# Kernel tuning notes

Hardware: AMD Instinct MI355X
Metric: run time of the kernel (lower is better)

Reference implementation:

```python
import jax, jax.numpy as jnp
import numpy as np

N = 1000000
E = 16000000


def gcn_conv(x, W, b, src, dst, dinv_sqrt):
    # x: [N, Cin]; W: [Cin, Cout]; src/dst: [E'] (self-loops included)
    xw = x @ W                                   # [N, Cout]
    norm = dinv_sqrt[src] * dinv_sqrt[dst]       # [E']
    msg = xw[src] * norm[:, None]                # [E', Cout]
    out = jax.ops.segment_sum(msg, dst, num_segments=x.shape[0])
    return out + b


def setup_inputs() -> dict:
    key = jax.random.key(0)
    ks = jax.random.split(key, 8)
    x = jax.random.normal(ks[0], (N, 1), dtype=jnp.float32)
    edge_index = jax.random.randint(ks[1], (2, E), 0, N, dtype=jnp.int64)
    W1 = jax.random.normal(ks[2], (1, 3), dtype=jnp.float32)
    b1 = jax.random.normal(ks[3], (3,), dtype=jnp.float32) * 0.1
    W2 = jax.random.normal(ks[4], (3, 3), dtype=jnp.float32) * 0.5
    b2 = jax.random.normal(ks[5], (3,), dtype=jnp.float32) * 0.1
    W3 = jax.random.normal(ks[6], (3, 3), dtype=jnp.float32) * 0.5
    b3 = jax.random.normal(ks[7], (3,), dtype=jnp.float32) * 0.1
    return {"x": x, "edge_index": edge_index, "W1": W1, "b1": b1,
            "W2": W2, "b2": b2, "W3": W3, "b3": b3}


def reference(x, edge_index, W1, b1, W2, b2, W3, b3):
    n = x.shape[0]
    # add self-loops (PyG GCNConv default)
    loop = jnp.arange(n, dtype=edge_index.dtype)
    src = jnp.concatenate([edge_index[0], loop])
    dst = jnp.concatenate([edge_index[1], loop])
    # symmetric normalization: deg over targets of A + I
    deg = jax.ops.segment_sum(jnp.ones_like(dst, dtype=x.dtype), dst, num_segments=n)
    dinv_sqrt = jnp.where(deg > 0, jax.lax.rsqrt(deg), 0.0)
    h = jax.nn.relu(gcn_conv(x, W1, b1, src, dst, dinv_sqrt))
    h = jax.nn.relu(gcn_conv(h, W2, b2, src, dst, dinv_sqrt))
    h = jax.nn.relu(gcn_conv(h, W3, b3, src, dst, dinv_sqrt))
    return h
```

## Files before the change

kernel.cpp:

```cpp
#include <hip/hip_runtime.h>

#define THREADS 256
#define SCAN_TPB 256
#define SCAN_ELEMS 4096
#define CHUNK 16384
#define BUCKET_BITS 10
#define BUCKET_SIZE 1024
#define MAXBUCK 4096

__device__ __forceinline__ long long llmin(long long a, long long b) { return a < b ? a : b; }


__global__ void detect_i64_kernel(const int* __restrict__ e, int* __restrict__ flag) {
    if (blockIdx.x == 0 && threadIdx.x == 0) {
        bool all_odd_zero = true, any_even = false;
#pragma unroll
        for (int k = 0; k < 16; ++k) {
            if (e[2 * k + 1] != 0) all_odd_zero = false;
            if (e[2 * k] != 0) any_even = true;
        }
        *flag = (all_odd_zero && any_even) ? 1 : 0;
    }
}


__global__ void hist_kernel(const int* __restrict__ e, long long E,
                            const int* __restrict__ flag,
                            int nchunks, int nbuck, int* __restrict__ H) {
    __shared__ int hist[MAXBUCK];
    for (int b = threadIdx.x; b < nbuck; b += blockDim.x) hist[b] = 0;
    __syncthreads();
    const bool i64 = (*flag != 0);
    long long beg = (long long)blockIdx.x * CHUNK;
    long long end = llmin(beg + CHUNK, E);
    if (i64) {
        const int2* d = (const int2*)e + E;
        for (long long i = beg + threadIdx.x; i < end; i += blockDim.x)
            atomicAdd(&hist[d[i].x >> BUCKET_BITS], 1);
    } else {
        const int* d = e + E;
        for (long long i = beg + threadIdx.x; i < end; i += blockDim.x)
            atomicAdd(&hist[d[i] >> BUCKET_BITS], 1);
    }
    __syncthreads();
    for (int b = threadIdx.x; b < nbuck; b += blockDim.x)
        H[(size_t)b * nchunks + blockIdx.x] = hist[b];
}

__global__ void scan1_kernel(const int* __restrict__ v, int len, int* __restrict__ bsum) {
    __shared__ int sh[SCAN_TPB];
    int base = blockIdx.x * SCAN_ELEMS + threadIdx.x * 16;
    int s = 0;
#pragma unroll
    for (int k = 0; k < 16; ++k) {
        int idx = base + k;
        if (idx < len) s += v[idx];
    }
    sh[threadIdx.x] = s;
    __syncthreads();
    for (int off = SCAN_TPB >> 1; off > 0; off >>= 1) {
        if (threadIdx.x < off) sh[threadIdx.x] += sh[threadIdx.x + off];
        __syncthreads();
    }
    if (threadIdx.x == 0) bsum[blockIdx.x] = sh[0];
}

__global__ void scan2_kernel(int* __restrict__ bsum, int nb) {
    if (blockIdx.x == 0 && threadIdx.x == 0) {
        int run = 0;
        for (int b = 0; b < nb; ++b) { int t = bsum[b]; bsum[b] = run; run += t; }
    }
}

__global__ void scan3_kernel(int* __restrict__ v, int len, const int* __restrict__ bsum) {
    __shared__ int sh[SCAN_TPB];
    int base = blockIdx.x * SCAN_ELEMS + threadIdx.x * 16;
    int vals[16];
    int mySum = 0;
#pragma unroll
    for (int k = 0; k < 16; ++k) {
        int idx = base + k;
        vals[k] = (idx < len) ? v[idx] : 0;
        mySum += vals[k];
    }
    sh[threadIdx.x] = mySum;
    __syncthreads();
    for (int off = 1; off < SCAN_TPB; off <<= 1) {
        int t = (threadIdx.x >= off) ? sh[threadIdx.x - off] : 0;
        __syncthreads();
        sh[threadIdx.x] += t;
        __syncthreads();
    }
    int run = bsum[blockIdx.x] + sh[threadIdx.x] - mySum;
#pragma unroll
    for (int k = 0; k < 16; ++k) {
        int idx = base + k;
        if (idx < len) { v[idx] = run; run += vals[k]; }
    }
}

__global__ void bstart_kernel(const int* __restrict__ H, int nchunks, int nbuck,
                              long long E, int* __restrict__ bs) {
    int b = blockIdx.x * blockDim.x + threadIdx.x;
    if (b < nbuck) bs[b] = H[(size_t)b * nchunks];
    if (b == 0) bs[nbuck] = (int)E;
}

__global__ void scatter_pack_kernel(const int* __restrict__ e, long long E,
                                    const int* __restrict__ flag,
                                    int nchunks, int nbuck, const int* __restrict__ H,
                                    int* __restrict__ packed) {
    __shared__ int cur[MAXBUCK];
    for (int b = threadIdx.x; b < nbuck; b += blockDim.x)
        cur[b] = H[(size_t)b * nchunks + blockIdx.x];
    __syncthreads();
    const bool i64 = (*flag != 0);
    long long beg = (long long)blockIdx.x * CHUNK;
    long long end = llmin(beg + CHUNK, E);
    for (long long i = beg + threadIdx.x; i < end; i += blockDim.x) {
        int s, t;
        if (i64) { s = ((const int2*)e)[i].x; t = ((const int2*)e)[E + i].x; }
        else     { s = e[i];                  t = e[E + i]; }
        int b = t >> BUCKET_BITS;
        int pos = atomicAdd(&cur[b], 1);
        packed[pos] = ((t & (BUCKET_SIZE - 1)) << 20) | s;
    }
}


__global__ void deg_init_kernel(const int* __restrict__ bs, const int* __restrict__ packed,
                                const float* __restrict__ x,
                                float* __restrict__ dinv, float* __restrict__ p, int N) {
    __shared__ int cnt[BUCKET_SIZE];
    for (int k = threadIdx.x; k < BUCKET_SIZE; k += blockDim.x) cnt[k] = 0;
    __syncthreads();
    int beg = bs[blockIdx.x], end = bs[blockIdx.x + 1];
    for (int k = beg + threadIdx.x; k < end; k += blockDim.x)
        atomicAdd(&cnt[((unsigned)packed[k]) >> 20], 1);
    __syncthreads();
    int base = blockIdx.x << BUCKET_BITS;
    for (int k = threadIdx.x; k < BUCKET_SIZE; k += blockDim.x) {
        int i = base + k;
        if (i < N) {
            float di = rsqrtf((float)cnt[k] + 1.0f);
            dinv[i] = di;
            p[i] = x[i] * di;
        }
    }
}

__global__ void layer1_bucket_kernel(const int* __restrict__ bs, const int* __restrict__ packed,
                                     const float* __restrict__ p, const float* __restrict__ dinv,
                                     const float* __restrict__ W1, const float* __restrict__ b1,
                                     const float* __restrict__ W2,
                                     float4* __restrict__ y2, int N) {
    __shared__ float acc[BUCKET_SIZE];
    for (int k = threadIdx.x; k < BUCKET_SIZE; k += blockDim.x) acc[k] = 0.0f;
    __syncthreads();
    int beg = bs[blockIdx.x], end = bs[blockIdx.x + 1];
    for (int k = beg + threadIdx.x; k < end; k += blockDim.x) {
        unsigned rec = (unsigned)packed[k];
        atomicAdd(&acc[rec >> 20], p[rec & 0xFFFFFu]);
    }
    __syncthreads();
    int base = blockIdx.x << BUCKET_BITS;
    for (int k = threadIdx.x; k < BUCKET_SIZE; k += blockDim.x) {
        int i = base + k;
        if (i >= N) continue;
        float di = dinv[i];
        float t = di * (acc[k] + p[i]);
        float h0 = fmaxf(t * W1[0] + b1[0], 0.0f);
        float h1 = fmaxf(t * W1[1] + b1[1], 0.0f);
        float h2 = fmaxf(t * W1[2] + b1[2], 0.0f);
        float4 o;
        o.x = di * (h0 * W2[0] + h1 * W2[3] + h2 * W2[6]);
        o.y = di * (h0 * W2[1] + h1 * W2[4] + h2 * W2[7]);
        o.z = di * (h0 * W2[2] + h1 * W2[5] + h2 * W2[8]);
        o.w = 0.0f;
        y2[i] = o;
    }
}

__global__ void layer_mid_bucket_kernel(const int* __restrict__ bs, const int* __restrict__ packed,
                                        const float4* __restrict__ y, const float* __restrict__ dinv,
                                        const float* __restrict__ b, const float* __restrict__ Wn,
                                        float4* __restrict__ ynext, int N) {
    __shared__ float acc[BUCKET_SIZE * 3];
    for (int k = threadIdx.x; k < BUCKET_SIZE * 3; k += blockDim.x) acc[k] = 0.0f;
    __syncthreads();
    int beg = bs[blockIdx.x], end = bs[blockIdx.x + 1];
    for (int k = beg + threadIdx.x; k < end; k += blockDim.x) {
        unsigned rec = (unsigned)packed[k];
        float4 v = y[rec & 0xFFFFFu];
        int dl = (rec >> 20) * 3;
        atomicAdd(&acc[dl + 0], v.x);
        atomicAdd(&acc[dl + 1], v.y);
        atomicAdd(&acc[dl + 2], v.z);
    }
    __syncthreads();
    int base = blockIdx.x << BUCKET_BITS;
    for (int k = threadIdx.x; k < BUCKET_SIZE; k += blockDim.x) {
        int i = base + k;
        if (i >= N) continue;
        float di = dinv[i];
        float4 yi = y[i];
        float h0 = fmaxf(di * (acc[k * 3 + 0] + yi.x) + b[0], 0.0f);
        float h1 = fmaxf(di * (acc[k * 3 + 1] + yi.y) + b[1], 0.0f);
        float h2 = fmaxf(di * (acc[k * 3 + 2] + yi.z) + b[2], 0.0f);
        float4 o;
        o.x = di * (h0 * Wn[0] + h1 * Wn[3] + h2 * Wn[6]);
        o.y = di * (h0 * Wn[1] + h1 * Wn[4] + h2 * Wn[7]);
        o.z = di * (h0 * Wn[2] + h1 * Wn[5] + h2 * Wn[8]);
        o.w = 0.0f;
        ynext[i] = o;
    }
}

__global__ void layer_last_bucket_kernel(const int* __restrict__ bs, const int* __restrict__ packed,
                                         const float4* __restrict__ y, const float* __restrict__ dinv,
                                         const float* __restrict__ b,
                                         float* __restrict__ out, int N) {
    __shared__ float acc[BUCKET_SIZE * 3];
    for (int k = threadIdx.x; k < BUCKET_SIZE * 3; k += blockDim.x) acc[k] = 0.0f;
    __syncthreads();
    int beg = bs[blockIdx.x], end = bs[blockIdx.x + 1];
    for (int k = beg + threadIdx.x; k < end; k += blockDim.x) {
        unsigned rec = (unsigned)packed[k];
        float4 v = y[rec & 0xFFFFFu];
        int dl = (rec >> 20) * 3;
        atomicAdd(&acc[dl + 0], v.x);
        atomicAdd(&acc[dl + 1], v.y);
        atomicAdd(&acc[dl + 2], v.z);
    }
    __syncthreads();
    int base = blockIdx.x << BUCKET_BITS;
    for (int k = threadIdx.x; k < BUCKET_SIZE; k += blockDim.x) {
        int i = base + k;
        if (i >= N) continue;
        float di = dinv[i];
        float4 yi = y[i];
        out[i * 3 + 0] = fmaxf(di * (acc[k * 3 + 0] + yi.x) + b[0], 0.0f);
        out[i * 3 + 1] = fmaxf(di * (acc[k * 3 + 1] + yi.y) + b[1], 0.0f);
        out[i * 3 + 2] = fmaxf(di * (acc[k * 3 + 2] + yi.z) + b[2], 0.0f);
    }
}


__global__ void deg_kernel(const int* __restrict__ e, long long E,
                           const int* __restrict__ flag, float* __restrict__ deg) {
    const bool i64 = (*flag != 0);
    long long i = (long long)blockIdx.x * blockDim.x + threadIdx.x;
    const long long stride = (long long)gridDim.x * blockDim.x;
    for (; i < E; i += stride) {
        long long t = i64 ? (long long)e[2 * E + 2 * i] : (long long)e[E + i];
        atomicAdd(deg + t, 1.0f);
    }
}

__global__ void node_init_kernel(const float* __restrict__ x, const float* __restrict__ W1,
                                 float* __restrict__ deg_dinv, float* __restrict__ A, int N) {
    int i = blockIdx.x * blockDim.x + threadIdx.x;
    if (i >= N) return;
    float di = rsqrtf(deg_dinv[i] + 1.0f);
    deg_dinv[i] = di;
    float v = x[i] * di;
    A[i * 3 + 0] = v * W1[0];
    A[i * 3 + 1] = v * W1[1];
    A[i * 3 + 2] = v * W1[2];
}

__global__ void scatter_kernel(const int* __restrict__ e, long long E,
                               const int* __restrict__ flag,
                               const float* __restrict__ y, float* __restrict__ acc) {
    const bool i64 = (*flag != 0);
    long long i = (long long)blockIdx.x * blockDim.x + threadIdx.x;
    const long long stride = (long long)gridDim.x * blockDim.x;
    for (; i < E; i += stride) {
        int s, t;
        if (i64) { s = e[2 * i]; t = e[2 * E + 2 * i]; }
        else     { s = e[i];     t = e[E + i]; }
        atomicAdd(acc + (long long)t * 3 + 0, y[(long long)s * 3 + 0]);
        atomicAdd(acc + (long long)t * 3 + 1, y[(long long)s * 3 + 1]);
        atomicAdd(acc + (long long)t * 3 + 2, y[(long long)s * 3 + 2]);
    }
}

__global__ void finalize_mid_kernel(const float* __restrict__ dinv, const float* __restrict__ y,
                                    float* __restrict__ acc, const float* __restrict__ b,
                                    const float* __restrict__ Wn, int N) {
    int i = blockIdx.x * blockDim.x + threadIdx.x;
    if (i >= N) return;
    float di = dinv[i];
    float h0 = fmaxf(di * (acc[i * 3 + 0] + y[i * 3 + 0]) + b[0], 0.0f);
    float h1 = fmaxf(di * (acc[i * 3 + 1] + y[i * 3 + 1]) + b[1], 0.0f);
    float h2 = fmaxf(di * (acc[i * 3 + 2] + y[i * 3 + 2]) + b[2], 0.0f);
    float z0 = di * (h0 * Wn[0] + h1 * Wn[3] + h2 * Wn[6]);
    float z1 = di * (h0 * Wn[1] + h1 * Wn[4] + h2 * Wn[7]);
    float z2 = di * (h0 * Wn[2] + h1 * Wn[5] + h2 * Wn[8]);
    acc[i * 3 + 0] = z0;
    acc[i * 3 + 1] = z1;
    acc[i * 3 + 2] = z2;
}

__global__ void finalize_last_kernel(const float* __restrict__ dinv, const float* __restrict__ y,
                                     const float* __restrict__ acc, const float* __restrict__ b,
                                     float* __restrict__ out, int N) {
    int i = blockIdx.x * blockDim.x + threadIdx.x;
    if (i >= N) return;
    float di = dinv[i];
    out[i * 3 + 0] = fmaxf(di * (acc[i * 3 + 0] + y[i * 3 + 0]) + b[0], 0.0f);
    out[i * 3 + 1] = fmaxf(di * (acc[i * 3 + 1] + y[i * 3 + 1]) + b[1], 0.0f);
    out[i * 3 + 2] = fmaxf(di * (acc[i * 3 + 2] + y[i * 3 + 2]) + b[2], 0.0f);
}


extern "C" void kernel_launch(void* const* d_in, const int* in_sizes, int n_in,
                              void* d_out, int out_size, void* d_ws, size_t ws_size,
                              hipStream_t stream) {
    const float* x  = (const float*)d_in[0];
    const int*   ei = (const int*)d_in[1];
    const float* W1 = (const float*)d_in[2];
    const float* b1 = (const float*)d_in[3];
    const float* W2 = (const float*)d_in[4];
    const float* b2 = (const float*)d_in[5];
    const float* W3 = (const float*)d_in[6];
    const float* b3 = (const float*)d_in[7];
    float* out = (float*)d_out;

    const long long N = in_sizes[0];
    const long long E = (long long)in_sizes[1] / 2;

    const int nbuck   = (int)((N + BUCKET_SIZE - 1) >> BUCKET_BITS);
    const int nchunks = (int)((E + CHUNK - 1) / CHUNK);
    const int len     = nbuck * nchunks;

    char* w = (char*)d_ws;
    size_t off = 0;
    auto alloc = [&](size_t bytes) -> char* {
        char* pp = w + off;
        off = (off + bytes + 255) & ~(size_t)255;
        return pp;
    };

    int*    flag   = (int*)alloc(4);
    int*    H      = (int*)alloc((size_t)len * 4);
    int*    bs     = (int*)alloc(((size_t)nbuck + 1) * 4);
    int*    packed = (int*)alloc((size_t)E * 4);
    float*  dinv   = (float*)alloc((size_t)N * 4);
    float*  p      = (float*)alloc((size_t)N * 4);
    float4* y2     = (float4*)alloc((size_t)N * 16);
    float4* y3     = (float4*)alloc((size_t)N * 16);

    const int nblk    = (int)((N + THREADS - 1) / THREADS);
    const int nb_scan = (len + SCAN_ELEMS - 1) / SCAN_ELEMS;

    if (off <= ws_size && N <= (1 << 20) && nbuck <= MAXBUCK) {
        detect_i64_kernel<<<1, 64, 0, stream>>>(ei, flag);
        hist_kernel<<<nchunks, THREADS, 0, stream>>>(ei, E, flag, nchunks, nbuck, H);
        int* bsum = (int*)p;
        scan1_kernel<<<nb_scan, SCAN_TPB, 0, stream>>>(H, len, bsum);
        scan2_kernel<<<1, 64, 0, stream>>>(bsum, nb_scan);
        scan3_kernel<<<nb_scan, SCAN_TPB, 0, stream>>>(H, len, bsum);
        bstart_kernel<<<(nbuck + THREADS) / THREADS, THREADS, 0, stream>>>(H, nchunks, nbuck, E, bs);
        scatter_pack_kernel<<<nchunks, THREADS, 0, stream>>>(ei, E, flag, nchunks, nbuck, H, packed);

        deg_init_kernel<<<nbuck, THREADS, 0, stream>>>(bs, packed, x, dinv, p, (int)N);
        layer1_bucket_kernel<<<nbuck, THREADS, 0, stream>>>(bs, packed, p, dinv, W1, b1, W2, y2, (int)N);
        layer_mid_bucket_kernel<<<nbuck, THREADS, 0, stream>>>(bs, packed, y2, dinv, b2, W3, y3, (int)N);
        layer_last_bucket_kernel<<<nbuck, THREADS, 0, stream>>>(bs, packed, y3, dinv, b3, out, (int)N);
    } else {
        int*   fflag = (int*)w;
        float* fdinv = (float*)(w + 256);
        float* A     = fdinv + N;
        size_t need_full = 256 + (size_t)N * 4 + (size_t)N * 12 * 2;
        float* B = (ws_size >= need_full) ? (A + 3 * N) : out;
        const int eblk = 2048;

        detect_i64_kernel<<<1, 64, 0, stream>>>(ei, fflag);
        hipMemsetAsync(fdinv, 0, (size_t)N * 4, stream);
        deg_kernel<<<eblk, THREADS, 0, stream>>>(ei, E, fflag, fdinv);
        node_init_kernel<<<nblk, THREADS, 0, stream>>>(x, W1, fdinv, A, (int)N);

        hipMemsetAsync(B, 0, (size_t)N * 12, stream);
        scatter_kernel<<<eblk, THREADS, 0, stream>>>(ei, E, fflag, A, B);
        finalize_mid_kernel<<<nblk, THREADS, 0, stream>>>(fdinv, A, B, b1, W2, (int)N);

        hipMemsetAsync(A, 0, (size_t)N * 12, stream);
        scatter_kernel<<<eblk, THREADS, 0, stream>>>(ei, E, fflag, B, A);
        finalize_mid_kernel<<<nblk, THREADS, 0, stream>>>(fdinv, B, A, b2, W3, (int)N);

        hipMemsetAsync(B, 0, (size_t)N * 12, stream);
        scatter_kernel<<<eblk, THREADS, 0, stream>>>(ei, E, fflag, A, B);
        finalize_last_kernel<<<nblk, THREADS, 0, stream>>>(fdinv, A, B, b3, out, (int)N);
    }
}
```

Measured before the change: 894.2 us.

## Replace global counting sort with per-tile shared-memory bin sort and segment offsets

The global histogram, three-pass scan, bucket-start and scattered pack kernels are replaced by one kernel. Each 8192-edge tile is bin-sorted by destination bucket in shared memory and written out contiguously, along with per-tile bucket offsets, which are then transposed. The aggregation kernels walk, for each bucket, its short segment in every tile instead of one contiguous range. This removes the scan launches and the random 4-byte global scatter writes. In exchange the layer passes do many short, divergent, serial segment reads per thread, which coalesce less well than the old contiguous ranges.

```diff
diff --git a/kernel.cpp b/kernel.cpp
--- a/kernel.cpp
+++ b/kernel.cpp
@@ -1,12 +1,11 @@
 #include <hip/hip_runtime.h>
 
 #define THREADS 256
-#define SCAN_TPB 256
-#define SCAN_ELEMS 4096
-#define CHUNK 16384
+#define TILE 8192
+#define TPB_S 512
+#define EPT 16
 #define BUCKET_BITS 10
 #define BUCKET_SIZE 1024
-#define MAXBUCK 4096
 
 __device__ __forceinline__ long long llmin(long long a, long long b) { return a < b ? a : b; }
 
@@ -24,122 +23,111 @@
 }
 
 
-__global__ void hist_kernel(const int* __restrict__ e, long long E,
-                            const int* __restrict__ flag,
-                            int nchunks, int nbuck, int* __restrict__ H) {
-    __shared__ int hist[MAXBUCK];
-    for (int b = threadIdx.x; b < nbuck; b += blockDim.x) hist[b] = 0;
-    __syncthreads();
+__global__ __launch_bounds__(TPB_S) void binsort_kernel(
+        const int* __restrict__ e, long long E, const int* __restrict__ flag,
+        int nbuck, int* __restrict__ packed, int* __restrict__ ofs) {
+    __shared__ int hist[1024];
+    __shared__ int sarr[TPB_S];
+    __shared__ int srec[TILE];
+    const int tid = threadIdx.x;
+    hist[tid] = 0;
+    hist[tid + TPB_S] = 0;
+    __syncthreads();
+
     const bool i64 = (*flag != 0);
-    long long beg = (long long)blockIdx.x * CHUNK;
-    long long end = llmin(beg + CHUNK, E);
-    if (i64) {
-        const int2* d = (const int2*)e + E;
-        for (long long i = beg + threadIdx.x; i < end; i += blockDim.x)
-            atomicAdd(&hist[d[i].x >> BUCKET_BITS], 1);
-    } else {
-        const int* d = e + E;
-        for (long long i = beg + threadIdx.x; i < end; i += blockDim.x)
-            atomicAdd(&hist[d[i] >> BUCKET_BITS], 1);
-    }
-    __syncthreads();
-    for (int b = threadIdx.x; b < nbuck; b += blockDim.x)
-        H[(size_t)b * nchunks + blockIdx.x] = hist[b];
-}
-
-__global__ void scan1_kernel(const int* __restrict__ v, int len, int* __restrict__ bsum) {
-    __shared__ int sh[SCAN_TPB];
-    int base = blockIdx.x * SCAN_ELEMS + threadIdx.x * 16;
-    int s = 0;
+    const long long beg = (long long)blockIdx.x * TILE;
+    const int tile_len = (int)llmin((long long)TILE, E - beg);
+
+    int rec[EPT];
+    int bkt[EPT];
 #pragma unroll
-    for (int k = 0; k < 16; ++k) {
-        int idx = base + k;
-        if (idx < len) s += v[idx];
-    }
-    sh[threadIdx.x] = s;
-    __syncthreads();
-    for (int off = SCAN_TPB >> 1; off > 0; off >>= 1) {
-        if (threadIdx.x < off) sh[threadIdx.x] += sh[threadIdx.x + off];
+    for (int k = 0; k < EPT; ++k) {
+        int j = tid + k * TPB_S;
+        bkt[k] = -1;
+        if (j < tile_len) {
+            long long idx = beg + j;
+            int s, d;
+            if (i64) { s = ((const int2*)e)[idx].x; d = ((const int2*)e)[E + idx].x; }
+            else     { s = e[idx];                  d = e[E + idx]; }
+            bkt[k] = d >> BUCKET_BITS;
+            rec[k] = ((d & (BUCKET_SIZE - 1)) << 20) | s;
+            atomicAdd(&hist[bkt[k]], 1);
+        }
+    }
+    __syncthreads();
+
+    int v0 = hist[2 * tid], v1 = hist[2 * tid + 1];
+    sarr[tid] = v0 + v1;
+    __syncthreads();
+    for (int off = 1; off < TPB_S; off <<= 1) {
+        int t = (tid >= off) ? sarr[tid - off] : 0;
         __syncthreads();
-    }
-    if (threadIdx.x == 0) bsum[blockIdx.x] = sh[0];
-}
-
-__global__ void scan2_kernel(int* __restrict__ bsum, int nb) {
-    if (blockIdx.x == 0 && threadIdx.x == 0) {
-        int run = 0;
-        for (int b = 0; b < nb; ++b) { int t = bsum[b]; bsum[b] = run; run += t; }
-    }
-}
-
-__global__ void scan3_kernel(int* __restrict__ v, int len, const int* __restrict__ bsum) {
-    __shared__ int sh[SCAN_TPB];
-    int base = blockIdx.x * SCAN_ELEMS + threadIdx.x * 16;
-    int vals[16];
-    int mySum = 0;
+        sarr[tid] += t;
+        __syncthreads();
+    }
+    int excl = (tid == 0) ? 0 : sarr[tid - 1];
+    hist[2 * tid] = excl;
+    hist[2 * tid + 1] = excl + v0;
+    __syncthreads();
+
+    int* orow = ofs + (size_t)blockIdx.x * nbuck;
+    if (tid < nbuck) orow[tid] = hist[tid];
+    if (tid + TPB_S < nbuck) orow[tid + TPB_S] = hist[tid + TPB_S];
+    __syncthreads();
+
 #pragma unroll
-    for (int k = 0; k < 16; ++k) {
-        int idx = base + k;
-        vals[k] = (idx < len) ? v[idx] : 0;
-        mySum += vals[k];
-    }
-    sh[threadIdx.x] = mySum;
-    __syncthreads();
-    for (int off = 1; off < SCAN_TPB; off <<= 1) {
-        int t = (threadIdx.x >= off) ? sh[threadIdx.x - off] : 0;
-        __syncthreads();
-        sh[threadIdx.x] += t;
-        __syncthreads();
-    }
-    int run = bsum[blockIdx.x] + sh[threadIdx.x] - mySum;
-#pragma unroll
-    for (int k = 0; k < 16; ++k) {
-        int idx = base + k;
-        if (idx < len) { v[idx] = run; run += vals[k]; }
-    }
-}
-
-__global__ void bstart_kernel(const int* __restrict__ H, int nchunks, int nbuck,
-                              long long E, int* __restrict__ bs) {
-    int b = blockIdx.x * blockDim.x + threadIdx.x;
-    if (b < nbuck) bs[b] = H[(size_t)b * nchunks];
-    if (b == 0) bs[nbuck] = (int)E;
-}
-
-__global__ void scatter_pack_kernel(const int* __restrict__ e, long long E,
-                                    const int* __restrict__ flag,
-                                    int nchunks, int nbuck, const int* __restrict__ H,
-                                    int* __restrict__ packed) {
-    __shared__ int cur[MAXBUCK];
-    for (int b = threadIdx.x; b < nbuck; b += blockDim.x)
-        cur[b] = H[(size_t)b * nchunks + blockIdx.x];
-    __syncthreads();
-    const bool i64 = (*flag != 0);
-    long long beg = (long long)blockIdx.x * CHUNK;
-    long long end = llmin(beg + CHUNK, E);
-    for (long long i = beg + threadIdx.x; i < end; i += blockDim.x) {
-        int s, t;
-        if (i64) { s = ((const int2*)e)[i].x; t = ((const int2*)e)[E + i].x; }
-        else     { s = e[i];                  t = e[E + i]; }
-        int b = t >> BUCKET_BITS;
-        int pos = atomicAdd(&cur[b], 1);
-        packed[pos] = ((t & (BUCKET_SIZE - 1)) << 20) | s;
-    }
-}
-
-
-__global__ void deg_init_kernel(const int* __restrict__ bs, const int* __restrict__ packed,
-                                const float* __restrict__ x,
-                                float* __restrict__ dinv, float* __restrict__ p, int N) {
+    for (int k = 0; k < EPT; ++k) {
+        if (bkt[k] >= 0) {
+            int pos = atomicAdd(&hist[bkt[k]], 1);
+            srec[pos] = rec[k];
+        }
+    }
+    __syncthreads();
+
+    int* prow = packed + (size_t)blockIdx.x * TILE;
+    for (int j = tid; j < tile_len; j += TPB_S) prow[j] = srec[j];
+}
+
+#define TRT 32
+__global__ void transpose_kernel(const int* __restrict__ in, int rows, int cols,
+                                 int* __restrict__ outT) {
+    __shared__ int tb[TRT][TRT + 1];
+    int c0 = blockIdx.x * TRT, r0 = blockIdx.y * TRT;
+    int lx = threadIdx.x, ly = threadIdx.y;
+    for (int dy = ly; dy < TRT; dy += 8) {
+        int r = r0 + dy, c = c0 + lx;
+        if (r < rows && c < cols) tb[dy][lx] = in[(size_t)r * cols + c];
+    }
+    __syncthreads();
+    for (int dy = ly; dy < TRT; dy += 8) {
+        int r = c0 + dy, c = r0 + lx;
+        if (r < cols && c < rows) outT[(size_t)r * rows + c] = tb[lx][dy];
+    }
+}
+
+
+__global__ __launch_bounds__(TPB_S) void deg_init_kernel(
+        const int* __restrict__ ofsT, const int* __restrict__ packed,
+        const float* __restrict__ x, long long E, int ntiles, int nbuck,
+        float* __restrict__ dinv, float* __restrict__ p, int N) {
     __shared__ int cnt[BUCKET_SIZE];
-    for (int k = threadIdx.x; k < BUCKET_SIZE; k += blockDim.x) cnt[k] = 0;
-    __syncthreads();
-    int beg = bs[blockIdx.x], end = bs[blockIdx.x + 1];
-    for (int k = beg + threadIdx.x; k < end; k += blockDim.x)
-        atomicAdd(&cnt[((unsigned)packed[k]) >> 20], 1);
-    __syncthreads();
-    int base = blockIdx.x << BUCKET_BITS;
-    for (int k = threadIdx.x; k < BUCKET_SIZE; k += blockDim.x) {
+    const int tid = threadIdx.x, b = blockIdx.x;
+    for (int k = tid; k < BUCKET_SIZE; k += TPB_S) cnt[k] = 0;
+    __syncthreads();
+    const int* row0 = ofsT + (size_t)b * ntiles;
+    const int* row1 = row0 + ntiles;
+    const bool last_b = (b == nbuck - 1);
+    for (int t = tid; t < ntiles; t += TPB_S) {
+        int o = row0[t];
+        int tl = (t == ntiles - 1) ? (int)(E - (long long)t * TILE) : TILE;
+        int o2 = last_b ? tl : row1[t];
+        const int* pr = packed + (size_t)t * TILE;
+        for (int j = o; j < o2; ++j)
+            atomicAdd(&cnt[((unsigned)pr[j]) >> 20], 1);
+    }
+    __syncthreads();
+    int base = b << BUCKET_BITS;
+    for (int k = tid; k < BUCKET_SIZE; k += TPB_S) {
         int i = base + k;
         if (i < N) {
             float di = rsqrtf((float)cnt[k] + 1.0f);
@@ -149,22 +137,32 @@
     }
 }
 
-__global__ void layer1_bucket_kernel(const int* __restrict__ bs, const int* __restrict__ packed,
-                                     const float* __restrict__ p, const float* __restrict__ dinv,
-                                     const float* __restrict__ W1, const float* __restrict__ b1,
-                                     const float* __restrict__ W2,
-                                     float4* __restrict__ y2, int N) {
+__global__ __launch_bounds__(TPB_S) void layer1_kernel(
+        const int* __restrict__ ofsT, const int* __restrict__ packed,
+        const float* __restrict__ p, const float* __restrict__ dinv,
+        const float* __restrict__ W1, const float* __restrict__ b1,
+        const float* __restrict__ W2, long long E, int ntiles, int nbuck,
+        float4* __restrict__ y2, int N) {
     __shared__ float acc[BUCKET_SIZE];
-    for (int k = threadIdx.x; k < BUCKET_SIZE; k += blockDim.x) acc[k] = 0.0f;
-    __syncthreads();
-    int beg = bs[blockIdx.x], end = bs[blockIdx.x + 1];
-    for (int k = beg + threadIdx.x; k < end; k += blockDim.x) {
-        unsigned rec = (unsigned)packed[k];
-        atomicAdd(&acc[rec >> 20], p[rec & 0xFFFFFu]);
-    }
-    __syncthreads();
-    int base = blockIdx.x << BUCKET_BITS;
-    for (int k = threadIdx.x; k < BUCKET_SIZE; k += blockDim.x) {
+    const int tid = threadIdx.x, b = blockIdx.x;
+    for (int k = tid; k < BUCKET_SIZE; k += TPB_S) acc[k] = 0.0f;
+    __syncthreads();
+    const int* row0 = ofsT + (size_t)b * ntiles;
+    const int* row1 = row0 + ntiles;
+    const bool last_b = (b == nbuck - 1);
+    for (int t = tid; t < ntiles; t += TPB_S) {
+        int o = row0[t];
+        int tl = (t == ntiles - 1) ? (int)(E - (long long)t * TILE) : TILE;
+        int o2 = last_b ? tl : row1[t];
+        const int* pr = packed + (size_t)t * TILE;
+        for (int j = o; j < o2; ++j) {
+            unsigned r = (unsigned)pr[j];
+            atomicAdd(&acc[r >> 20], p[r & 0xFFFFFu]);
+        }
+    }
+    __syncthreads();
+    int base = b << BUCKET_BITS;
+    for (int k = tid; k < BUCKET_SIZE; k += TPB_S) {
         int i = base + k;
         if (i >= N) continue;
         float di = dinv[i];
@@ -181,32 +179,43 @@
     }
 }
 
-__global__ void layer_mid_bucket_kernel(const int* __restrict__ bs, const int* __restrict__ packed,
-                                        const float4* __restrict__ y, const float* __restrict__ dinv,
-                                        const float* __restrict__ b, const float* __restrict__ Wn,
-                                        float4* __restrict__ ynext, int N) {
+__global__ __launch_bounds__(TPB_S) void layer_mid_kernel(
+        const int* __restrict__ ofsT, const int* __restrict__ packed,
+        const float4* __restrict__ y, const float* __restrict__ dinv,
+        const float* __restrict__ bb, const float* __restrict__ Wn,
+        long long E, int ntiles, int nbuck,
+        float4* __restrict__ ynext, int N) {
     __shared__ float acc[BUCKET_SIZE * 3];
-    for (int k = threadIdx.x; k < BUCKET_SIZE * 3; k += blockDim.x) acc[k] = 0.0f;
-    __syncthreads();
-    int beg = bs[blockIdx.x], end = bs[blockIdx.x + 1];
-    for (int k = beg + threadIdx.x; k < end; k += blockDim.x) {
-        unsigned rec = (unsigned)packed[k];
-        float4 v = y[rec & 0xFFFFFu];
-        int dl = (rec >> 20) * 3;
-        atomicAdd(&acc[dl + 0], v.x);
-        atomicAdd(&acc[dl + 1], v.y);
-        atomicAdd(&acc[dl + 2], v.z);
-    }
-    __syncthreads();
-    int base = blockIdx.x << BUCKET_BITS;
-    for (int k = threadIdx.x; k < BUCKET_SIZE; k += blockDim.x) {
+    const int tid = threadIdx.x, b = blockIdx.x;
+    for (int k = tid; k < BUCKET_SIZE * 3; k += TPB_S) acc[k] = 0.0f;
+    __syncthreads();
+    const int* row0 = ofsT + (size_t)b * ntiles;
+    const int* row1 = row0 + ntiles;
+    const bool last_b = (b == nbuck - 1);
+    for (int t = tid; t < ntiles; t += TPB_S) {
+        int o = row0[t];
+        int tl = (t == ntiles - 1) ? (int)(E - (long long)t * TILE) : TILE;
+        int o2 = last_b ? tl : row1[t];
+        const int* pr = packed + (size_t)t * TILE;
+        for (int j = o; j < o2; ++j) {
+            unsigned r = (unsigned)pr[j];
+            float4 v = y[r & 0xFFFFFu];
+            int dl = (r >> 20) * 3;
+            atomicAdd(&acc[dl + 0], v.x);
+            atomicAdd(&acc[dl + 1], v.y);
+            atomicAdd(&acc[dl + 2], v.z);
+        }
+    }
+    __syncthreads();
+    int base = b << BUCKET_BITS;
+    for (int k = tid; k < BUCKET_SIZE; k += TPB_S) {
         int i = base + k;
         if (i >= N) continue;
         float di = dinv[i];
         float4 yi = y[i];
-        float h0 = fmaxf(di * (acc[k * 3 + 0] + yi.x) + b[0], 0.0f);
-        float h1 = fmaxf(di * (acc[k * 3 + 1] + yi.y) + b[1], 0.0f);
-        float h2 = fmaxf(di * (acc[k * 3 + 2] + yi.z) + b[2], 0.0f);
+        float h0 = fmaxf(di * (acc[k * 3 + 0] + yi.x) + bb[0], 0.0f);
+        float h1 = fmaxf(di * (acc[k * 3 + 1] + yi.y) + bb[1], 0.0f);
+        float h2 = fmaxf(di * (acc[k * 3 + 2] + yi.z) + bb[2], 0.0f);
         float4 o;
         o.x = di * (h0 * Wn[0] + h1 * Wn[3] + h2 * Wn[6]);
         o.y = di * (h0 * Wn[1] + h1 * Wn[4] + h2 * Wn[7]);
@@ -216,32 +225,42 @@
     }
 }
 
-__global__ void layer_last_bucket_kernel(const int* __restrict__ bs, const int* __restrict__ packed,
-                                         const float4* __restrict__ y, const float* __restrict__ dinv,
-                                         const float* __restrict__ b,
-                                         float* __restrict__ out, int N) {
+__global__ __launch_bounds__(TPB_S) void layer_last_kernel(
+        const int* __restrict__ ofsT, const int* __restrict__ packed,
+        const float4* __restrict__ y, const float* __restrict__ dinv,
+        const float* __restrict__ bb, long long E, int ntiles, int nbuck,
+        float* __restrict__ out, int N) {
     __shared__ float acc[BUCKET_SIZE * 3];
-    for (int k = threadIdx.x; k < BUCKET_SIZE * 3; k += blockDim.x) acc[k] = 0.0f;
-    __syncthreads();
-    int beg = bs[blockIdx.x], end = bs[blockIdx.x + 1];
-    for (int k = beg + threadIdx.x; k < end; k += blockDim.x) {
-        unsigned rec = (unsigned)packed[k];
-        float4 v = y[rec & 0xFFFFFu];
-        int dl = (rec >> 20) * 3;
-        atomicAdd(&acc[dl + 0], v.x);
-        atomicAdd(&acc[dl + 1], v.y);
-        atomicAdd(&acc[dl + 2], v.z);
-    }
-    __syncthreads();
-    int base = blockIdx.x << BUCKET_BITS;
-    for (int k = threadIdx.x; k < BUCKET_SIZE; k += blockDim.x) {
+    const int tid = threadIdx.x, b = blockIdx.x;
+    for (int k = tid; k < BUCKET_SIZE * 3; k += TPB_S) acc[k] = 0.0f;
+    __syncthreads();
+    const int* row0 = ofsT + (size_t)b * ntiles;
+    const int* row1 = row0 + ntiles;
+    const bool last_b = (b == nbuck - 1);
+    for (int t = tid; t < ntiles; t += TPB_S) {
+        int o = row0[t];
+        int tl = (t == ntiles - 1) ? (int)(E - (long long)t * TILE) : TILE;
+        int o2 = last_b ? tl : row1[t];
+        const int* pr = packed + (size_t)t * TILE;
+        for (int j = o; j < o2; ++j) {
+            unsigned r = (unsigned)pr[j];
+            float4 v = y[r & 0xFFFFFu];
+            int dl = (r >> 20) * 3;
+            atomicAdd(&acc[dl + 0], v.x);
+            atomicAdd(&acc[dl + 1], v.y);
+            atomicAdd(&acc[dl + 2], v.z);
+        }
+    }
+    __syncthreads();
+    int base = b << BUCKET_BITS;
+    for (int k = tid; k < BUCKET_SIZE; k += TPB_S) {
         int i = base + k;
         if (i >= N) continue;
         float di = dinv[i];
         float4 yi = y[i];
-        out[i * 3 + 0] = fmaxf(di * (acc[k * 3 + 0] + yi.x) + b[0], 0.0f);
-        out[i * 3 + 1] = fmaxf(di * (acc[k * 3 + 1] + yi.y) + b[1], 0.0f);
-        out[i * 3 + 2] = fmaxf(di * (acc[k * 3 + 2] + yi.z) + b[2], 0.0f);
+        out[i * 3 + 0] = fmaxf(di * (acc[k * 3 + 0] + yi.x) + bb[0], 0.0f);
+        out[i * 3 + 1] = fmaxf(di * (acc[k * 3 + 1] + yi.y) + bb[1], 0.0f);
+        out[i * 3 + 2] = fmaxf(di * (acc[k * 3 + 2] + yi.z) + bb[2], 0.0f);
     }
 }
 
@@ -330,9 +349,8 @@
     const long long N = in_sizes[0];
     const long long E = (long long)in_sizes[1] / 2;
 
-    const int nbuck   = (int)((N + BUCKET_SIZE - 1) >> BUCKET_BITS);
-    const int nchunks = (int)((E + CHUNK - 1) / CHUNK);
-    const int len     = nbuck * nchunks;
+    const int nbuck  = (int)((N + BUCKET_SIZE - 1) >> BUCKET_BITS);
+    const int ntiles = (int)((E + TILE - 1) / TILE);
 
     char* w = (char*)d_ws;
     size_t off = 0;
@@ -343,31 +361,32 @@
     };
 
     int*    flag   = (int*)alloc(4);
-    int*    H      = (int*)alloc((size_t)len * 4);
-    int*    bs     = (int*)alloc(((size_t)nbuck + 1) * 4);
-    int*    packed = (int*)alloc((size_t)E * 4);
+    int*    ofsT   = (int*)alloc((size_t)nbuck * ntiles * 4);
+    int*    packed = (int*)alloc((size_t)ntiles * TILE * 4);
     float*  dinv   = (float*)alloc((size_t)N * 4);
     float*  p      = (float*)alloc((size_t)N * 4);
     float4* y2     = (float4*)alloc((size_t)N * 16);
     float4* y3     = (float4*)alloc((size_t)N * 16);
-
-    const int nblk    = (int)((N + THREADS - 1) / THREADS);
-    const int nb_scan = (len + SCAN_ELEMS - 1) / SCAN_ELEMS;
-
-    if (off <= ws_size && N <= (1 << 20) && nbuck <= MAXBUCK) {
+    int*    ofs    = (int*)y2;
+
+    const int nblk = (int)((N + THREADS - 1) / THREADS);
+
+    if (off <= ws_size && N <= (1 << 20) && nbuck <= 1024 &&
+        (size_t)nbuck * ntiles * 4 <= (size_t)N * 16) {
         detect_i64_kernel<<<1, 64, 0, stream>>>(ei, flag);
-        hist_kernel<<<nchunks, THREADS, 0, stream>>>(ei, E, flag, nchunks, nbuck, H);
-        int* bsum = (int*)p;
-        scan1_kernel<<<nb_scan, SCAN_TPB, 0, stream>>>(H, len, bsum);
-        scan2_kernel<<<1, 64, 0, stream>>>(bsum, nb_scan);
-        scan3_kernel<<<nb_scan, SCAN_TPB, 0, stream>>>(H, len, bsum);
-        bstart_kernel<<<(nbuck + THREADS) / THREADS, THREADS, 0, stream>>>(H, nchunks, nbuck, E, bs);
-        scatter_pack_kernel<<<nchunks, THREADS, 0, stream>>>(ei, E, flag, nchunks, nbuck, H, packed);
-
-        deg_init_kernel<<<nbuck, THREADS, 0, stream>>>(bs, packed, x, dinv, p, (int)N);
-        layer1_bucket_kernel<<<nbuck, THREADS, 0, stream>>>(bs, packed, p, dinv, W1, b1, W2, y2, (int)N);
-        layer_mid_bucket_kernel<<<nbuck, THREADS, 0, stream>>>(bs, packed, y2, dinv, b2, W3, y3, (int)N);
-        layer_last_bucket_kernel<<<nbuck, THREADS, 0, stream>>>(bs, packed, y3, dinv, b3, out, (int)N);
+        binsort_kernel<<<ntiles, TPB_S, 0, stream>>>(ei, E, flag, nbuck, packed, ofs);
+        dim3 tb(32, 8);
+        dim3 tg((nbuck + TRT - 1) / TRT, (ntiles + TRT - 1) / TRT);
+        transpose_kernel<<<tg, tb, 0, stream>>>(ofs, ntiles, nbuck, ofsT);
+
+        deg_init_kernel<<<nbuck, TPB_S, 0, stream>>>(ofsT, packed, x, E, ntiles, nbuck,
+                                                     dinv, p, (int)N);
+        layer1_kernel<<<nbuck, TPB_S, 0, stream>>>(ofsT, packed, p, dinv, W1, b1, W2,
+                                                   E, ntiles, nbuck, y2, (int)N);
+        layer_mid_kernel<<<nbuck, TPB_S, 0, stream>>>(ofsT, packed, y2, dinv, b2, W3,
+                                                      E, ntiles, nbuck, y3, (int)N);
+        layer_last_kernel<<<nbuck, TPB_S, 0, stream>>>(ofsT, packed, y3, dinv, b3,
+                                                       E, ntiles, nbuck, out, (int)N);
     } else {
         int*   fflag = (int*)w;
         float* fdinv = (float*)(w + 256);
```

Result: slower. 1.579 ms (+76.6%).
